# Performance work log

Hardware: AMD Instinct MI355X
Metric: run time of the kernel (lower is better)

Reference implementation:

```python
import jax, jax.numpy as jnp
import numpy as np

B, S, DIN, DOUT = 4, 2048, 4096, 4096

def setup_inputs() -> dict:
    key = jax.random.key(0)
    k1, k2, k3 = jax.random.split(key, 3)
    x = jax.random.normal(k1, (B, S, DIN), dtype=jnp.float32)
    # symmetric int8 quantized weights, [out_features, in_features]
    int_weight = jax.random.randint(k2, (DOUT, DIN), -128, 128, dtype=jnp.int32).astype(jnp.int8)
    w_scale = jnp.float32(0.01)  # per-tensor scale, zero-point = 0
    fp_bias = jax.random.normal(k3, (DOUT,), dtype=jnp.float32) * 0.01
    return {"x": x, "int_weight": int_weight, "w_scale": w_scale, "fp_bias": fp_bias}

def reference(x, int_weight, w_scale, fp_bias):
    # Dequantize weight: fp32 = int8 * scale (elementwise), then F.linear: x @ w.T + b
    w = int_weight.astype(jnp.float32) * w_scale  # [DOUT, DIN]
    out = jnp.einsum('bsi,oi->bso', x, w) + fp_bias
    return out
```

## Files before the change

kernel.cpp:

```cpp
#include <hip/hip_runtime.h>
#include <hip/hip_bf16.h>

typedef __attribute__((ext_vector_type(8))) short bf16x8;
typedef __attribute__((ext_vector_type(4))) float f32x4;
typedef __attribute__((ext_vector_type(4))) int i32x4;
typedef __attribute__((ext_vector_type(2))) unsigned int u32x2;
typedef __attribute__((ext_vector_type(4))) unsigned int u32x4;

__device__ __forceinline__ unsigned int f2bf(float f) {
    union { float f; unsigned int u; } v; v.f = f;
    unsigned int u = v.u;
    u += 0x7FFFu + ((u >> 16) & 1u);
    return u >> 16;
}

__device__ __forceinline__ void gl_lds16(const void* gptr, void* lptr) {
    __builtin_amdgcn_global_load_lds(
        (const __attribute__((address_space(1))) unsigned int*)gptr,
        (__attribute__((address_space(3))) unsigned int*)lptr, 16, 0, 0);
}

__global__ __launch_bounds__(256) void convert_xw_kernel(
    const float* __restrict__ x, const int* __restrict__ w,
    unsigned short* __restrict__ xb, unsigned short* __restrict__ wb,
    long long nx8, long long ntot8)
{
    long long i = (long long)blockIdx.x * blockDim.x + threadIdx.x;
    const long long stride = (long long)gridDim.x * blockDim.x;
    for (; i < ntot8; i += stride) {
        if (i < nx8) {
            const f32x4* p = (const f32x4*)(x + i * 8);
            f32x4 v0 = p[0], v1 = p[1];
            u32x4 q;
            q[0] = f2bf(v0[0]) | (f2bf(v0[1]) << 16);
            q[1] = f2bf(v0[2]) | (f2bf(v0[3]) << 16);
            q[2] = f2bf(v1[0]) | (f2bf(v1[1]) << 16);
            q[3] = f2bf(v1[2]) | (f2bf(v1[3]) << 16);
            *(u32x4*)(xb + i * 8) = q;
        } else {
            const long long j = i - nx8;
            const i32x4* p = (const i32x4*)(w + j * 8);
            i32x4 v0 = p[0], v1 = p[1];
            u32x4 q;
            q[0] = f2bf((float)v0[0]) | (f2bf((float)v0[1]) << 16);
            q[1] = f2bf((float)v0[2]) | (f2bf((float)v0[3]) << 16);
            q[2] = f2bf((float)v1[0]) | (f2bf((float)v1[1]) << 16);
            q[3] = f2bf((float)v1[2]) | (f2bf((float)v1[3]) << 16);
            *(u32x4*)(wb + j * 8) = q;
        }
    }
}

__global__ __launch_bounds__(512, 2) void gemm256_kernel(
    const unsigned short* __restrict__ A, const unsigned short* __restrict__ Bw,
    const float* __restrict__ wscale, const float* __restrict__ bias,
    float* __restrict__ out, int M, int N, int K)
{
    __shared__ unsigned char lds[163840];
    const int B0OFF = 98304;

    const int tid  = threadIdx.x;
    const int lane = tid & 63;
    const int wid  = tid >> 6;
    const int wr   = wid >> 1;
    const int wc   = wid & 1;

    const int ntn = N >> 8;
    const int nwg = gridDim.x;
    int bid = blockIdx.x;
    if ((nwg & 7) == 0) {
        const int cpx = nwg >> 3;
        bid = (bid & 7) * cpx + (bid >> 3);
    }
    const int bm = bid / ntn;
    const int bn = bid % ntn;
    const int NT = K >> 6;

    const char* Abase = (const char*)(A  + (size_t)bm * 256 * K);
    const char* Bbase = (const char*)(Bw + (size_t)bn * 256 * K);
    const size_t rowb = (size_t)K * 2;

    const int s_colb = (((lane & 7) ^ (lane >> 3)) << 4);
    const int s_rsub = wid * 8 + (lane >> 3);
    const int s_ldso = wid * 1024 + lane * 16;

    auto stageHalf = [&](const char* gRowBase, char* lhalf) {
#pragma unroll
        for (int q = 0; q < 2; ++q)
            gl_lds16(gRowBase + (size_t)(q * 64 + s_rsub) * rowb + s_colb,
                     lhalf + q * 8192 + s_ldso);
    };
    auto Ag = [&](int kt, int h) { return Abase + (size_t)kt * 128 + (size_t)(h * 128) * rowb; };
    auto Bg = [&](int kt, int h) { return Bbase + (size_t)kt * 128 + (size_t)(h * 128) * rowb; };

    const int arow = (wr * 64  + (lane & 15)) * 128;
    const int brow = (wc * 128 + (lane & 15)) * 128;
    const int csw0 = (((lane >> 4) * 16))      ^ ((lane & 7) << 4);
    const int csw1 = (((lane >> 4) * 16) + 64) ^ ((lane & 7) << 4);

    f32x4 acc[4][8];
#pragma unroll
    for (int mi = 0; mi < 4; ++mi)
#pragma unroll
        for (int ni = 0; ni < 8; ++ni)
            acc[mi][ni] = (f32x4){0.f, 0.f, 0.f, 0.f};

    bf16x8 a0[4], a1[4], bA[4], bB[4];

    stageHalf(Ag(0, 0), (char*)lds + 0);
    stageHalf(Ag(0, 1), (char*)lds + 16384);
    stageHalf(Bg(0, 0), (char*)lds + B0OFF);
    stageHalf(Bg(0, 1), (char*)lds + B0OFF + 16384);
    if (NT > 1) {
        stageHalf(Ag(1, 0), (char*)lds + 32768);
        stageHalf(Ag(1, 1), (char*)lds + 32768 + 16384);
        asm volatile("s_waitcnt vmcnt(4)" ::: "memory");
    } else {
        asm volatile("s_waitcnt vmcnt(0)" ::: "memory");
    }
    __builtin_amdgcn_sched_barrier(0);
    asm volatile("s_barrier" ::: "memory");
    {
        const char* Al = (const char*)lds;
        const char* Bl = (const char*)lds + B0OFF;
#pragma unroll
        for (int fm = 0; fm < 4; ++fm) a0[fm] = *(const bf16x8*)(Al + arow + fm * 2048 + csw0);
#pragma unroll
        for (int fn = 0; fn < 4; ++fn) bA[fn] = *(const bf16x8*)(Bl + brow + fn * 2048 + csw0);
    }

    int acur = 0, anxt = 32768, ann = 65536;
    int bcur = B0OFF, both = B0OFF + 32768;

    for (int kt = 0; kt < NT; ++kt) {
        const char* Al = (const char*)lds + acur;
        const char* Bl = (const char*)lds + bcur;
        char* Bs  = (char*)lds + both;
        char* As2 = (char*)lds + ann;

        if (kt + 1 < NT) stageHalf(Bg(kt + 1, 0), Bs);
#pragma unroll
        for (int fm = 0; fm < 4; ++fm) a1[fm] = *(const bf16x8*)(Al + arow + fm * 2048 + csw1);
#pragma unroll
        for (int fn = 0; fn < 4; ++fn) bB[fn] = *(const bf16x8*)(Bl + brow + (fn + 4) * 2048 + csw0);
        __builtin_amdgcn_s_setprio(1);
#pragma unroll
        for (int fm = 0; fm < 4; ++fm)
#pragma unroll
            for (int fn = 0; fn < 4; ++fn)
                acc[fm][fn] = __builtin_amdgcn_mfma_f32_16x16x32_bf16(a0[fm], bA[fn], acc[fm][fn], 0, 0, 0);
        __builtin_amdgcn_s_setprio(0);

        if (kt + 1 < NT) stageHalf(Bg(kt + 1, 1), Bs + 16384);
#pragma unroll
        for (int fn = 0; fn < 4; ++fn) bA[fn] = *(const bf16x8*)(Bl + brow + fn * 2048 + csw1);
        __builtin_amdgcn_s_setprio(1);
#pragma unroll
        for (int fm = 0; fm < 4; ++fm)
#pragma unroll
            for (int fn = 0; fn < 4; ++fn)
                acc[fm][fn + 4] = __builtin_amdgcn_mfma_f32_16x16x32_bf16(a0[fm], bB[fn], acc[fm][fn + 4], 0, 0, 0);
        __builtin_amdgcn_s_setprio(0);

        if (kt + 2 < NT) stageHalf(Ag(kt + 2, 0), As2);
#pragma unroll
        for (int fn = 0; fn < 4; ++fn) bB[fn] = *(const bf16x8*)(Bl + brow + (fn + 4) * 2048 + csw1);
        __builtin_amdgcn_s_setprio(1);
#pragma unroll
        for (int fm = 0; fm < 4; ++fm)
#pragma unroll
            for (int fn = 0; fn < 4; ++fn)
                acc[fm][fn] = __builtin_amdgcn_mfma_f32_16x16x32_bf16(a1[fm], bA[fn], acc[fm][fn], 0, 0, 0);
        __builtin_amdgcn_s_setprio(0);

        if (kt + 2 < NT) stageHalf(Ag(kt + 2, 1), As2 + 16384);
        if (kt + 1 < NT) {
            if (kt + 2 < NT) { asm volatile("s_waitcnt vmcnt(4)" ::: "memory"); }
            else             { asm volatile("s_waitcnt vmcnt(0)" ::: "memory"); }
            __builtin_amdgcn_sched_barrier(0);
            asm volatile("s_barrier" ::: "memory");
            const char* nAl = (const char*)lds + anxt;
            const char* nBl = (const char*)lds + both;
#pragma unroll
            for (int fm = 0; fm < 4; ++fm) a0[fm] = *(const bf16x8*)(nAl + arow + fm * 2048 + csw0);
#pragma unroll
            for (int fn = 0; fn < 4; ++fn) bA[fn] = *(const bf16x8*)(nBl + brow + fn * 2048 + csw0);
        }
        __builtin_amdgcn_s_setprio(1);
#pragma unroll
        for (int fm = 0; fm < 4; ++fm)
#pragma unroll
            for (int fn = 0; fn < 4; ++fn)
                acc[fm][fn + 4] = __builtin_amdgcn_mfma_f32_16x16x32_bf16(a1[fm], bB[fn], acc[fm][fn + 4], 0, 0, 0);
        __builtin_amdgcn_s_setprio(0);
        asm volatile("s_barrier" ::: "memory");

        const int at = acur; acur = anxt; anxt = ann; ann = at;
        const int bt = bcur; bcur = both; both = bt;
    }

    const float scale = *wscale;
    const int orow0 = bm * 256 + wr * 64  + ((lane >> 4) << 2);
    const int ocol0 = bn * 256 + wc * 128 + (lane & 15);
#pragma unroll
    for (int fn = 0; fn < 8; ++fn) {
        const int col = ocol0 + 16 * fn;
        const float bb = bias[col];
#pragma unroll
        for (int fm = 0; fm < 4; ++fm) {
            const int row0 = orow0 + 16 * fm;
#pragma unroll
            for (int i = 0; i < 4; ++i)
                out[(size_t)(row0 + i) * N + col] = acc[fm][fn][i] * scale + bb;
        }
    }
}

__device__ __forceinline__ int swz(int row, int byte_in_row) {
    return row * 128 + (byte_in_row ^ ((row & 7) << 4));
}

__global__ __launch_bounds__(256) void qlinear_fused_kernel(
    const float* __restrict__ X, const int* __restrict__ W,
    const float* __restrict__ wscale, const float* __restrict__ bias,
    float* __restrict__ out, int M, int N, int K)
{
    __shared__ unsigned char smem[32768];

    const int t    = threadIdx.x;
    const int lane = t & 63;
    const int wid  = t >> 6;
    const int wr   = wid >> 1;
    const int wc   = wid & 1;

    const int ntn = N >> 7;
    const int bm  = blockIdx.x / ntn;
    const int bn  = blockIdx.x % ntn;
    const int NT  = K >> 6;

    const float* Ab = X + (size_t)bm * 128 * K;
    const int*   Bb = W + (size_t)bn * 128 * K;

    const int srow = t >> 4, sc4 = t & 15;

    f32x4 av[8];
    i32x4 bv[8];

    auto loadAB = [&](int kt) {
        const float* Ap = Ab + kt * 64 + sc4 * 4;
#pragma unroll
        for (int l = 0; l < 8; ++l)
            av[l] = *(const f32x4*)(Ap + (size_t)(srow + 16 * l) * K);
        const int* Bp = Bb + kt * 64 + sc4 * 4;
#pragma unroll
        for (int l = 0; l < 8; ++l)
            bv[l] = *(const i32x4*)(Bp + (size_t)(srow + 16 * l) * K);
    };

    auto writeAB = [&]() {
#pragma unroll
        for (int l = 0; l < 8; ++l) {
            const int row = srow + 16 * l;
            u32x2 pk;
            pk[0] = f2bf(av[l][0]) | (f2bf(av[l][1]) << 16);
            pk[1] = f2bf(av[l][2]) | (f2bf(av[l][3]) << 16);
            *(u32x2*)(smem + swz(row, sc4 * 8)) = pk;
        }
#pragma unroll
        for (int l = 0; l < 8; ++l) {
            const int row = srow + 16 * l;
            u32x2 pk;
            pk[0] = f2bf((float)bv[l][0]) | (f2bf((float)bv[l][1]) << 16);
            pk[1] = f2bf((float)bv[l][2]) | (f2bf((float)bv[l][3]) << 16);
            *(u32x2*)(smem + 16384 + swz(row, sc4 * 8)) = pk;
        }
    };

    f32x4 acc[4][4];
#pragma unroll
    for (int mi = 0; mi < 4; ++mi)
#pragma unroll
        for (int ni = 0; ni < 4; ++ni)
            acc[mi][ni] = (f32x4){0.f, 0.f, 0.f, 0.f};

    const int kbyte = (lane >> 4) * 16;
    const int afr   = wr * 64 + (lane & 15);
    const int bfr   = wc * 64 + (lane & 15);

    loadAB(0);

    for (int kt = 0; kt < NT; ++kt) {
        writeAB();
        __syncthreads();
        if (kt + 1 < NT) loadAB(kt + 1);
#pragma unroll
        for (int kk = 0; kk < 2; ++kk) {
            bf16x8 a[4], b[4];
#pragma unroll
            for (int mi = 0; mi < 4; ++mi)
                a[mi] = *(const bf16x8*)(smem + swz(afr + 16 * mi, kk * 64 + kbyte));
#pragma unroll
            for (int ni = 0; ni < 4; ++ni)
                b[ni] = *(const bf16x8*)(smem + 16384 + swz(bfr + 16 * ni, kk * 64 + kbyte));
#pragma unroll
            for (int mi = 0; mi < 4; ++mi)
#pragma unroll
                for (int ni = 0; ni < 4; ++ni)
                    acc[mi][ni] = __builtin_amdgcn_mfma_f32_16x16x32_bf16(
                        a[mi], b[ni], acc[mi][ni], 0, 0, 0);
        }
        __syncthreads();
    }

    const float scale = *wscale;
    const int orow0 = bm * 128 + wr * 64 + ((lane >> 4) << 2);
    const int ocol0 = bn * 128 + wc * 64 + (lane & 15);
#pragma unroll
    for (int ni = 0; ni < 4; ++ni) {
        const int col = ocol0 + 16 * ni;
        const float bb = bias[col];
#pragma unroll
        for (int mi = 0; mi < 4; ++mi) {
            const int row0 = orow0 + 16 * mi;
#pragma unroll
            for (int i = 0; i < 4; ++i)
                out[(size_t)(row0 + i) * N + col] = acc[mi][ni][i] * scale + bb;
        }
    }
}

extern "C" void kernel_launch(void* const* d_in, const int* in_sizes, int n_in,
                              void* d_out, int out_size, void* d_ws, size_t ws_size,
                              hipStream_t stream) {
    const float* x      = (const float*)d_in[0];
    const int*   w      = (const int*)d_in[1];
    const float* wscale = (const float*)d_in[2];
    const float* bias   = (const float*)d_in[3];
    float*       out    = (float*)d_out;

    const int DOUT = in_sizes[3];
    const int DIN  = in_sizes[1] / DOUT;
    const int M    = in_sizes[0] / DIN;

    const size_t xb_bytes = (size_t)M * DIN * 2;
    const size_t wb_bytes = (size_t)DOUT * DIN * 2;

    if (ws_size >= xb_bytes + wb_bytes && (M % 256) == 0 && (DOUT % 256) == 0
        && (DIN % 64) == 0 && (DIN / 64) >= 2) {
        unsigned short* xb = (unsigned short*)d_ws;
        unsigned short* wb = (unsigned short*)((char*)d_ws + xb_bytes);

        const long long nx8 = (long long)M * DIN / 8;
        const long long nw8 = (long long)DOUT * DIN / 8;
        convert_xw_kernel<<<2048, 256, 0, stream>>>(x, w, xb, wb, nx8, nx8 + nw8);

        dim3 grid((M / 256) * (DOUT / 256));
        gemm256_kernel<<<grid, 512, 0, stream>>>(xb, wb, wscale, bias, out, M, DOUT, DIN);
    } else {
        dim3 grid((M / 128) * (DOUT / 128));
        qlinear_fused_kernel<<<grid, 256, 0, stream>>>(x, w, wscale, bias, out, M, DOUT, DIN);
    }
}
```

Before: 278.1 us.

## Use 4 waves per 256x256 tile with 128x128 warp tiles

The GEMM block shrinks from 8 waves to 4. Each wave now computes a 128x128 output sub-tile (8x8 MFMA fragments) instead of 64x128, so it reuses each LDS fragment across more MFMAs. Staging is reorganized so 256 threads issue 4 loads per half-tile, and the waitcnt thresholds are adjusted to match. The per-thread accumulator count doubles to 256 floats, which adds register pressure (possible spills, one block per CU) and leaves fewer waves to hide latency.

```diff
diff --git a/kernel.cpp b/kernel.cpp
--- a/kernel.cpp
+++ b/kernel.cpp
@@ -51,7 +51,7 @@
     }
 }
 
-__global__ __launch_bounds__(512, 2) void gemm256_kernel(
+__global__ __launch_bounds__(256, 1) void gemm256_kernel(
     const unsigned short* __restrict__ A, const unsigned short* __restrict__ Bw,
     const float* __restrict__ wscale, const float* __restrict__ bias,
     float* __restrict__ out, int M, int N, int K)
@@ -80,32 +80,32 @@
     const char* Bbase = (const char*)(Bw + (size_t)bn * 256 * K);
     const size_t rowb = (size_t)K * 2;
 
-    const int s_colb = (((lane & 7) ^ (lane >> 3)) << 4);
-    const int s_rsub = wid * 8 + (lane >> 3);
-    const int s_ldso = wid * 1024 + lane * 16;
+    const int s_colb = (((tid & 7) ^ ((tid >> 3) & 7)) << 4);
+    const int s_rsub = tid >> 3;
+    const int s_ldso = tid * 16;
 
     auto stageHalf = [&](const char* gRowBase, char* lhalf) {
 #pragma unroll
-        for (int q = 0; q < 2; ++q)
-            gl_lds16(gRowBase + (size_t)(q * 64 + s_rsub) * rowb + s_colb,
-                     lhalf + q * 8192 + s_ldso);
+        for (int p = 0; p < 4; ++p)
+            gl_lds16(gRowBase + (size_t)(p * 32 + s_rsub) * rowb + s_colb,
+                     lhalf + p * 4096 + s_ldso);
     };
     auto Ag = [&](int kt, int h) { return Abase + (size_t)kt * 128 + (size_t)(h * 128) * rowb; };
     auto Bg = [&](int kt, int h) { return Bbase + (size_t)kt * 128 + (size_t)(h * 128) * rowb; };
 
-    const int arow = (wr * 64  + (lane & 15)) * 128;
+    const int arow = (wr * 128 + (lane & 15)) * 128;
     const int brow = (wc * 128 + (lane & 15)) * 128;
     const int csw0 = (((lane >> 4) * 16))      ^ ((lane & 7) << 4);
     const int csw1 = (((lane >> 4) * 16) + 64) ^ ((lane & 7) << 4);
 
-    f32x4 acc[4][8];
-#pragma unroll
-    for (int mi = 0; mi < 4; ++mi)
+    f32x4 acc[8][8];
+#pragma unroll
+    for (int mi = 0; mi < 8; ++mi)
 #pragma unroll
         for (int ni = 0; ni < 8; ++ni)
             acc[mi][ni] = (f32x4){0.f, 0.f, 0.f, 0.f};
 
-    bf16x8 a0[4], a1[4], bA[4], bB[4];
+    bf16x8 aC[8], aN[8], bP[4], bQ[4];
 
     stageHalf(Ag(0, 0), (char*)lds + 0);
     stageHalf(Ag(0, 1), (char*)lds + 16384);
@@ -114,7 +114,7 @@
     if (NT > 1) {
         stageHalf(Ag(1, 0), (char*)lds + 32768);
         stageHalf(Ag(1, 1), (char*)lds + 32768 + 16384);
-        asm volatile("s_waitcnt vmcnt(4)" ::: "memory");
+        asm volatile("s_waitcnt vmcnt(8)" ::: "memory");
     } else {
         asm volatile("s_waitcnt vmcnt(0)" ::: "memory");
     }
@@ -124,9 +124,9 @@
         const char* Al = (const char*)lds;
         const char* Bl = (const char*)lds + B0OFF;
 #pragma unroll
-        for (int fm = 0; fm < 4; ++fm) a0[fm] = *(const bf16x8*)(Al + arow + fm * 2048 + csw0);
-#pragma unroll
-        for (int fn = 0; fn < 4; ++fn) bA[fn] = *(const bf16x8*)(Bl + brow + fn * 2048 + csw0);
+        for (int fm = 0; fm < 8; ++fm) aC[fm] = *(const bf16x8*)(Al + arow + fm * 2048 + csw0);
+#pragma unroll
+        for (int fn = 0; fn < 4; ++fn) bP[fn] = *(const bf16x8*)(Bl + brow + fn * 2048 + csw0);
     }
 
     int acur = 0, anxt = 32768, ann = 65536;
@@ -140,58 +140,58 @@
 
         if (kt + 1 < NT) stageHalf(Bg(kt + 1, 0), Bs);
 #pragma unroll
-        for (int fm = 0; fm < 4; ++fm) a1[fm] = *(const bf16x8*)(Al + arow + fm * 2048 + csw1);
-#pragma unroll
-        for (int fn = 0; fn < 4; ++fn) bB[fn] = *(const bf16x8*)(Bl + brow + (fn + 4) * 2048 + csw0);
+        for (int fn = 0; fn < 4; ++fn) bQ[fn] = *(const bf16x8*)(Bl + brow + (fn + 4) * 2048 + csw0);
         __builtin_amdgcn_s_setprio(1);
 #pragma unroll
-        for (int fm = 0; fm < 4; ++fm)
+        for (int fm = 0; fm < 8; ++fm)
 #pragma unroll
             for (int fn = 0; fn < 4; ++fn)
-                acc[fm][fn] = __builtin_amdgcn_mfma_f32_16x16x32_bf16(a0[fm], bA[fn], acc[fm][fn], 0, 0, 0);
+                acc[fm][fn] = __builtin_amdgcn_mfma_f32_16x16x32_bf16(aC[fm], bP[fn], acc[fm][fn], 0, 0, 0);
         __builtin_amdgcn_s_setprio(0);
 
         if (kt + 1 < NT) stageHalf(Bg(kt + 1, 1), Bs + 16384);
 #pragma unroll
-        for (int fn = 0; fn < 4; ++fn) bA[fn] = *(const bf16x8*)(Bl + brow + fn * 2048 + csw1);
+        for (int fm = 0; fm < 8; ++fm) aN[fm] = *(const bf16x8*)(Al + arow + fm * 2048 + csw1);
+#pragma unroll
+        for (int fn = 0; fn < 4; ++fn) bP[fn] = *(const bf16x8*)(Bl + brow + fn * 2048 + csw1);
         __builtin_amdgcn_s_setprio(1);
 #pragma unroll
-        for (int fm = 0; fm < 4; ++fm)
+        for (int fm = 0; fm < 8; ++fm)
 #pragma unroll
             for (int fn = 0; fn < 4; ++fn)
-                acc[fm][fn + 4] = __builtin_amdgcn_mfma_f32_16x16x32_bf16(a0[fm], bB[fn], acc[fm][fn + 4], 0, 0, 0);
+                acc[fm][fn + 4] = __builtin_amdgcn_mfma_f32_16x16x32_bf16(aC[fm], bQ[fn], acc[fm][fn + 4], 0, 0, 0);
         __builtin_amdgcn_s_setprio(0);
 
         if (kt + 2 < NT) stageHalf(Ag(kt + 2, 0), As2);
 #pragma unroll
-        for (int fn = 0; fn < 4; ++fn) bB[fn] = *(const bf16x8*)(Bl + brow + (fn + 4) * 2048 + csw1);
+        for (int fn = 0; fn < 4; ++fn) bQ[fn] = *(const bf16x8*)(Bl + brow + (fn + 4) * 2048 + csw1);
         __builtin_amdgcn_s_setprio(1);
 #pragma unroll
-        for (int fm = 0; fm < 4; ++fm)
+        for (int fm = 0; fm < 8; ++fm)
 #pragma unroll
             for (int fn = 0; fn < 4; ++fn)
-                acc[fm][fn] = __builtin_amdgcn_mfma_f32_16x16x32_bf16(a1[fm], bA[fn], acc[fm][fn], 0, 0, 0);
+                acc[fm][fn] = __builtin_amdgcn_mfma_f32_16x16x32_bf16(aN[fm], bP[fn], acc[fm][fn], 0, 0, 0);
         __builtin_amdgcn_s_setprio(0);
 
         if (kt + 2 < NT) stageHalf(Ag(kt + 2, 1), As2 + 16384);
         if (kt + 1 < NT) {
-            if (kt + 2 < NT) { asm volatile("s_waitcnt vmcnt(4)" ::: "memory"); }
+            if (kt + 2 < NT) { asm volatile("s_waitcnt vmcnt(8)" ::: "memory"); }
             else             { asm volatile("s_waitcnt vmcnt(0)" ::: "memory"); }
             __builtin_amdgcn_sched_barrier(0);
             asm volatile("s_barrier" ::: "memory");
             const char* nAl = (const char*)lds + anxt;
             const char* nBl = (const char*)lds + both;
 #pragma unroll
-            for (int fm = 0; fm < 4; ++fm) a0[fm] = *(const bf16x8*)(nAl + arow + fm * 2048 + csw0);
-#pragma unroll
-            for (int fn = 0; fn < 4; ++fn) bA[fn] = *(const bf16x8*)(nBl + brow + fn * 2048 + csw0);
+            for (int fm = 0; fm < 8; ++fm) aC[fm] = *(const bf16x8*)(nAl + arow + fm * 2048 + csw0);
+#pragma unroll
+            for (int fn = 0; fn < 4; ++fn) bP[fn] = *(const bf16x8*)(nBl + brow + fn * 2048 + csw0);
         }
         __builtin_amdgcn_s_setprio(1);
 #pragma unroll
-        for (int fm = 0; fm < 4; ++fm)
+        for (int fm = 0; fm < 8; ++fm)
 #pragma unroll
             for (int fn = 0; fn < 4; ++fn)
-                acc[fm][fn + 4] = __builtin_amdgcn_mfma_f32_16x16x32_bf16(a1[fm], bB[fn], acc[fm][fn + 4], 0, 0, 0);
+                acc[fm][fn + 4] = __builtin_amdgcn_mfma_f32_16x16x32_bf16(aN[fm], bQ[fn], acc[fm][fn + 4], 0, 0, 0);
         __builtin_amdgcn_s_setprio(0);
         asm volatile("s_barrier" ::: "memory");
 
@@ -200,14 +200,14 @@
     }
 
     const float scale = *wscale;
-    const int orow0 = bm * 256 + wr * 64  + ((lane >> 4) << 2);
+    const int orow0 = bm * 256 + wr * 128 + ((lane >> 4) << 2);
     const int ocol0 = bn * 256 + wc * 128 + (lane & 15);
 #pragma unroll
     for (int fn = 0; fn < 8; ++fn) {
         const int col = ocol0 + 16 * fn;
         const float bb = bias[col];
 #pragma unroll
-        for (int fm = 0; fm < 4; ++fm) {
+        for (int fm = 0; fm < 8; ++fm) {
             const int row0 = orow0 + 16 * fm;
 #pragma unroll
             for (int i = 0; i < 4; ++i)
@@ -355,7 +355,7 @@
         convert_xw_kernel<<<2048, 256, 0, stream>>>(x, w, xb, wb, nx8, nx8 + nw8);
 
         dim3 grid((M / 256) * (DOUT / 256));
-        gemm256_kernel<<<grid, 512, 0, stream>>>(xb, wb, wscale, bias, out, M, DOUT, DIN);
+        gemm256_kernel<<<grid, 256, 0, stream>>>(xb, wb, wscale, bias, out, M, DOUT, DIN);
     } else {
         dim3 grid((M / 128) * (DOUT / 128));
         qlinear_fused_kernel<<<grid, 256, 0, stream>>>(x, w, wscale, bias, out, M, DOUT, DIN);
```

Measured after the change: 304.4 us. +9.4%, slower.
